# Performance work log

Hardware: AMD Instinct MI355X
Metric: run time of the kernel (lower is better)

## Reference

```python
import jax, jax.numpy as jnp
import numpy as np

# Model dims (match init_kwargs)
B, S, IN = 8, 96, 128          # batch, seq_len, control+data bits
H, M, N = 2, 32, 512           # heads, memory content size, memory addresses
STATE, OUT, NS = 256, 126, 3   # hidden state, output (data bits), shift size
EPS = 1e-12
# per-head interface parameter layout: s, jd, j, gamma, erase, add, k, beta, g
_SPLITS = [NS, 1, 3, 1, M, M, M, 1, 1]
_OFFS = np.concatenate([[0], np.cumsum(_SPLITS)])


def setup_inputs() -> dict:
    key = jax.random.key(0)
    ks = jax.random.split(key, 4)
    CIN = IN + H * M + STATE  # controller input: x ++ read ++ state
    return {
        "x": jax.random.normal(ks[0], (B, S, IN), jnp.float32),
        "W_s": jax.random.normal(ks[1], (CIN, STATE), jnp.float32) * 0.05,
        "b_s": jnp.zeros((STATE,), jnp.float32),
        "W_o": jax.random.normal(ks[2], (CIN, OUT), jnp.float32) * 0.05,
        "b_o": jnp.zeros((OUT,), jnp.float32),
        "W_u": jax.random.normal(ks[3], (CIN, int(_OFFS[-1]) * H), jnp.float32) * 0.05,
        "b_u": jnp.zeros((int(_OFFS[-1]) * H,), jnp.float32),
    }


def _circular_conv(wt, s):
    # wt: [B,H,N], s: [B,H,NS] softmax shift kernel centered at 0
    out = jnp.zeros_like(wt)
    c = NS // 2
    for i in range(NS):
        out = out + s[..., i:i + 1] * jnp.roll(wt, shift=i - c, axis=-1)
    return out


def _dwm_forward(x, W_s, b_s, W_o, b_o, W_u, b_u):
    b = x.shape[0]
    state0 = jnp.ones((b, STATE), x.dtype)
    wt0 = jnp.zeros((b, H, N), x.dtype).at[:, :, 0].set(1.0)
    mem0 = jnp.full((b, M, N), 0.01, x.dtype)

    def step(carry, x_t):
        state, wt, wt_dyn, mem = carry
        # ---- read: attention over memory addresses ----
        read = jnp.einsum('bhn,bmn->bhm', wt, mem).reshape(b, H * M)
        comb = jnp.concatenate([x_t, read, state], axis=-1)
        # ---- controller ----
        state_n = jax.nn.sigmoid(comb @ W_s + b_s)
        out_t = comb @ W_o + b_o
        upd = (comb @ W_u + b_u).reshape(b, H, int(_OFFS[-1]))
        sp = [upd[..., int(_OFFS[i]):int(_OFFS[i + 1])] for i in range(len(_SPLITS))]
        s, jd, j, gamma, erase, add, k, beta, g = sp
        s = jax.nn.softmax(jax.nn.softplus(s), axis=-1)
        jd = jax.nn.sigmoid(jd)
        j = jax.nn.softmax(j, axis=-1)
        gamma = 1.0 + jax.nn.softplus(gamma)
        erase = jax.nn.sigmoid(erase)
        k = jnp.tanh(k)
        beta = jax.nn.softplus(beta)
        g = jax.nn.sigmoid(g)
        # ---- memory write (erase then add, NTM-style multi-head) ----
        mem = mem * jnp.prod(1.0 - erase[:, :, :, None] * wt[:, :, None, :], axis=1)
        mem = mem + jnp.einsum('bhm,bhn->bmn', add, wt)
        # ---- content addressing (cosine similarity) ----
        k_n = k / (jnp.linalg.norm(k, axis=-1, keepdims=True) + EPS)
        m_n = mem / (jnp.linalg.norm(mem, axis=1, keepdims=True) + EPS)
        wt_k = jnp.einsum('bhm,bmn->bhn', k_n, m_n)
        wt_c = g * jax.nn.softmax(beta * wt_k, axis=-1) + (1.0 - g) * wt
        # ---- shift + sharpen + renormalize ----
        wt_sh = (_circular_conv(wt_c, s) + EPS) ** gamma
        wt_n = wt_sh / jnp.sum(wt_sh, axis=-1, keepdims=True)
        # ---- bookmark (snapshot) update + jump interpolation ----
        wt_a0 = jnp.zeros_like(wt_n).at[..., 0].set(1.0)
        wt_dyn_n = (1.0 - jd) * wt_dyn + jd * wt_n
        wt_f = j[..., 0:1] * wt_n + j[..., 1:2] * wt_a0 + j[..., 2:3] * wt_dyn
        return (state_n, wt_f, wt_dyn_n, mem), out_t

    _, outs = jax.lax.scan(step, (state0, wt0, wt0, mem0), jnp.swapaxes(x, 0, 1))
    return jnp.swapaxes(outs, 0, 1)  # [B, S, OUT]


def reference(x, W_s, b_s, W_o, b_o, W_u, b_u):
    return _dwm_forward(x, W_s, b_s, W_o, b_o, W_u, b_u)
```

## Files before the change

### kernel.cpp

```cpp
#include <hip/hip_runtime.h>
#include <math.h>

#define NTHREADS 1024

namespace {
constexpr int kB = 8, kS = 96, kIN = 128, kH = 2, kM = 32, kN = 512;
constexpr int kSTATE = 256, kOUT = 126, kUH = 106;
constexpr int kNC = 594;
constexpr int kKR = 320;
constexpr int kMLD = 520;
constexpr float kEPS = 1e-12f;
constexpr int kXWfloats = kB * kS * kNC;
constexpr size_t kWbOffBytes = (size_t)kXWfloats * 4;
}

__device__ __forceinline__ float sigm_(float x) { return 1.0f / (1.0f + __expf(-x)); }
__device__ __forceinline__ float splus_(float x) { return x > 20.0f ? x : __logf(1.0f + __expf(x)); }
__device__ __forceinline__ float blo_(unsigned int u) { return __uint_as_float(u << 16); }
__device__ __forceinline__ float bhi_(unsigned int u) { return __uint_as_float(u & 0xffff0000u); }

__global__ __launch_bounds__(640) void prep_xw(
    const float* __restrict__ x,
    const float* __restrict__ Ws, const float* __restrict__ bs,
    const float* __restrict__ Wo, const float* __restrict__ bo,
    const float* __restrict__ Wu, const float* __restrict__ bu,
    float* __restrict__ xw)
{
    __shared__ float sx[kIN];
    const int row = blockIdx.x;
    const int t = threadIdx.x;
    if (t < kIN) sx[t] = x[row * kIN + t];
    __syncthreads();
    if (t < kNC) {
        const float* Wp; int ld, j; float acc;
        if (t < 256)      { Wp = Ws; ld = kSTATE;   j = t;       acc = bs[j]; }
        else if (t < 382) { Wp = Wo; ld = kOUT;     j = t - 256; acc = bo[j]; }
        else              { Wp = Wu; ld = kH * kUH; j = t - 382; acc = bu[j]; }
        const float* p = Wp + j;
        #pragma unroll 8
        for (int i = 0; i < kIN; ++i) acc = fmaf(sx[i], p[i * ld], acc);
        xw[row * kNC + t] = acc;
    }
}

__global__ __launch_bounds__(1024) void prep_pack(
    const float* __restrict__ Ws, const float* __restrict__ Wo,
    const float* __restrict__ Wu, unsigned short* __restrict__ Wb)
{
    int idx = blockIdx.x * 1024 + threadIdx.x;
    if (idx >= kKR * kNC) return;
    int i = idx / kNC, c = idx - i * kNC;
    float v;
    if (c < 256)      v = Ws[(kIN + i) * kSTATE + c];
    else if (c < 382) v = Wo[(kIN + i) * kOUT + (c - 256)];
    else              v = Wu[(kIN + i) * (kH * kUH) + (c - 382)];
    unsigned int bits = __float_as_uint(v);
    unsigned int r = (bits + 0x7fffu + ((bits >> 16) & 1u)) >> 16;
    Wb[idx] = (unsigned short)r;
}

__global__ __launch_bounds__(NTHREADS) void dwm_kernel(
    const float* __restrict__ xw,
    const unsigned int* __restrict__ Wb,
    float* __restrict__ out)
{
    __shared__ float s_mem[kM * kMLD];
    __shared__ float s_wt[kH * kN];
    __shared__ float s_wtd[kH * kN];
    __shared__ float s_tmp[kH * kN];
    __shared__ float s_comb[320];
    __shared__ float s_upd[kH * kUH];
    __shared__ float s_er[kH * kM], s_ad[kH * kM], s_kk[kH * kM];
    __shared__ float s_red[16];
    __shared__ float s_shift[kH][3], s_jmp[kH][3];
    __shared__ float s_jd[kH], s_gam[kH], s_beta[kH], s_g[kH], s_ikn[kH];

    const int b = blockIdx.x;
    const int t = threadIdx.x;
    const int wid = t >> 6;
    const int lane = t & 63;

    for (int i = t; i < kM * kN; i += NTHREADS)
        s_mem[(i >> 9) * kMLD + (i & 511)] = 0.01f;
    for (int i = t; i < kH * kN; i += NTHREADS) {
        float v = ((i & 511) == 0) ? 1.0f : 0.0f;
        s_wt[i] = v; s_wtd[i] = v;
    }
    if (t < kSTATE) s_comb[64 + t] = 1.0f;
    __syncthreads();

    for (int step = 0; step < kS; ++step) {
        {
            int g = t >> 4, l16 = t & 15, h = g >> 5, m = g & 31;
            const float4* w4 = (const float4*)&s_wt[h * kN];
            const float4* m4 = (const float4*)&s_mem[m * kMLD];
            float ax = 0.0f, ay = 0.0f, az = 0.0f, aw = 0.0f;
            #pragma unroll
            for (int k = 0; k < 8; ++k) {
                float4 w = w4[l16 + 16 * k];
                float4 mv = m4[l16 + 16 * k];
                ax = fmaf(w.x, mv.x, ax); ay = fmaf(w.y, mv.y, ay);
                az = fmaf(w.z, mv.z, az); aw = fmaf(w.w, mv.w, aw);
            }
            float acc = (ax + ay) + (az + aw);
            acc += __shfl_xor(acc, 1);
            acc += __shfl_xor(acc, 2);
            acc += __shfl_xor(acc, 4);
            acc += __shfl_xor(acc, 8);
            if (l16 == 0) s_comb[g] = acc;
        }
        __syncthreads();

        float a0 = 0.0f, a1 = 0.0f;
        if (t < 297) {
            const unsigned int* wp = Wb + t;
            const float* xr = &xw[(b * kS + step) * kNC + 2 * t];
            a0 = xr[0]; a1 = xr[1];
            #pragma unroll 16
            for (int i = 0; i < kKR; ++i) {
                unsigned int u = wp[i * 297];
                float c = s_comb[i];
                a0 = fmaf(blo_(u), c, a0);
                a1 = fmaf(bhi_(u), c, a1);
            }
        }
        __syncthreads();

        if (t < 297) {
            int c0 = 2 * t;
            if (c0 < kSTATE) {
                s_comb[64 + c0] = sigm_(a0);
                s_comb[65 + c0] = sigm_(a1);
            } else if (c0 < kSTATE + kOUT) {
                float* o = &out[(b * kS + step) * kOUT];
                o[c0 - 256] = a0; o[c0 - 255] = a1;
            } else {
                int i0 = c0 - 382;
                auto disp = [&](int idx, float v) {
                    int h = idx >= kUH;
                    int j = idx - (h ? kUH : 0);
                    if (j >= 8 && j < 40)        s_er[h * kM + j - 8]  = sigm_(v);
                    else if (j >= 40 && j < 72)  s_ad[h * kM + j - 40] = v;
                    else if (j >= 72 && j < 104) s_kk[h * kM + j - 72] = tanhf(v);
                    else s_upd[idx] = v;
                };
                disp(i0, a0);
                disp(i0 + 1, a1);
            }
        }
        __syncthreads();

        if (t < 64) {
            int h = t >> 5, m = t & 31;
            float kv = s_kk[t];
            float ss = kv * kv;
            ss += __shfl_xor(ss, 1);
            ss += __shfl_xor(ss, 2);
            ss += __shfl_xor(ss, 4);
            ss += __shfl_xor(ss, 8);
            ss += __shfl_xor(ss, 16);
            if (m == 0) s_ikn[h] = 1.0f / (sqrtf(ss) + kEPS);
        } else if (t == 64 || t == 65) {
            int h = t - 64;
            const float* u = &s_upd[h * kUH];
            float b0 = splus_(u[0]), b1 = splus_(u[1]), b2 = splus_(u[2]);
            float mx = fmaxf(b0, fmaxf(b1, b2));
            float e0 = __expf(b0 - mx), e1 = __expf(b1 - mx), e2 = __expf(b2 - mx);
            float inv = 1.0f / (e0 + e1 + e2);
            s_shift[h][0] = e0 * inv; s_shift[h][1] = e1 * inv; s_shift[h][2] = e2 * inv;
            s_jd[h] = sigm_(u[3]);
            b0 = u[4]; b1 = u[5]; b2 = u[6];
            mx = fmaxf(b0, fmaxf(b1, b2));
            e0 = __expf(b0 - mx); e1 = __expf(b1 - mx); e2 = __expf(b2 - mx);
            inv = 1.0f / (e0 + e1 + e2);
            s_jmp[h][0] = e0 * inv; s_jmp[h][1] = e1 * inv; s_jmp[h][2] = e2 * inv;
            s_gam[h]  = 1.0f + splus_(u[7]);
            s_beta[h] = splus_(u[104]);
            s_g[h]    = sigm_(u[105]);
        }
        {
            int tn = t & 127, tm = t >> 7;
            int n0 = tn << 2;
            float4 w0v = *(const float4*)&s_wt[n0];
            float4 w1v = *(const float4*)&s_wt[kN + n0];
            #pragma unroll
            for (int r = 0; r < 4; ++r) {
                int m = tm + (r << 3);
                float er0 = s_er[m], er1 = s_er[kM + m];
                float ad0 = s_ad[m], ad1 = s_ad[kM + m];
                float4* mp = (float4*)&s_mem[m * kMLD + n0];
                float4 v = *mp;
                v.x = v.x * (1.0f - er0 * w0v.x) * (1.0f - er1 * w1v.x) + ad0 * w0v.x + ad1 * w1v.x;
                v.y = v.y * (1.0f - er0 * w0v.y) * (1.0f - er1 * w1v.y) + ad0 * w0v.y + ad1 * w1v.y;
                v.z = v.z * (1.0f - er0 * w0v.z) * (1.0f - er1 * w1v.z) + ad0 * w0v.z + ad1 * w1v.z;
                v.w = v.w * (1.0f - er0 * w0v.w) * (1.0f - er1 * w1v.w) + ad0 * w0v.w + ad1 * w1v.w;
                *mp = v;
            }
        }
        __syncthreads();

        if (t < kN) {
            int n = t;
            float c0 = 0.0f, c1 = 0.0f, ss = 0.0f;
            #pragma unroll
            for (int m = 0; m < kM; ++m) {
                float v = s_mem[m * kMLD + n];
                c0 = fmaf(s_kk[m], v, c0);
                c1 = fmaf(s_kk[kM + m], v, c1);
                ss = fmaf(v, v, ss);
            }
            float invc = 1.0f / (sqrtf(ss) + kEPS);
            float e0 = __expf(s_beta[0] * (c0 * s_ikn[0] * invc));
            float e1 = __expf(s_beta[1] * (c1 * s_ikn[1] * invc));
            s_tmp[n]      = e0;
            s_tmp[kN + n] = e1;
            float sm0 = e0, sm1 = e1;
            sm0 += __shfl_xor(sm0, 1);  sm1 += __shfl_xor(sm1, 1);
            sm0 += __shfl_xor(sm0, 2);  sm1 += __shfl_xor(sm1, 2);
            sm0 += __shfl_xor(sm0, 4);  sm1 += __shfl_xor(sm1, 4);
            sm0 += __shfl_xor(sm0, 8);  sm1 += __shfl_xor(sm1, 8);
            sm0 += __shfl_xor(sm0, 16); sm1 += __shfl_xor(sm1, 16);
            sm0 += __shfl_xor(sm0, 32); sm1 += __shfl_xor(sm1, 32);
            if (lane == 0) { s_red[wid] = sm0; s_red[8 + wid] = sm1; }
        }
        __syncthreads();

        {
            int h = t >> 9;
            float tot = 0.0f;
            #pragma unroll
            for (int i = 0; i < 8; ++i) tot += s_red[h * 8 + i];
            float e = s_tmp[t];
            float wc = s_g[h] * e / tot + (1.0f - s_g[h]) * s_wt[t];
            s_tmp[t] = wc;
        }
        __syncthreads();

        {
            int h = t >> 9, n = t & 511;
            const float* wcp = &s_tmp[h * kN];
            float cv = s_shift[h][0] * wcp[(n + 1) & 511]
                     + s_shift[h][1] * wcp[n]
                     + s_shift[h][2] * wcp[(n + 511) & 511];
            float wsh = exp2f(s_gam[h] * __log2f(cv + kEPS));
            float sm = wsh;
            sm += __shfl_xor(sm, 1);
            sm += __shfl_xor(sm, 2);
            sm += __shfl_xor(sm, 4);
            sm += __shfl_xor(sm, 8);
            sm += __shfl_xor(sm, 16);
            sm += __shfl_xor(sm, 32);
            if (lane == 0) s_red[wid] = sm;
            __syncthreads();
            float tot = 0.0f;
            #pragma unroll
            for (int i = 0; i < 8; ++i) tot += s_red[h * 8 + i];
            float wn = wsh / tot;
            float dold = s_wtd[t];
            s_wtd[t] = (1.0f - s_jd[h]) * dold + s_jd[h] * wn;
            float wa0 = (n == 0) ? 1.0f : 0.0f;
            s_wt[t] = s_jmp[h][0] * wn + s_jmp[h][1] * wa0 + s_jmp[h][2] * dold;
        }
        __syncthreads();
    }
}

extern "C" void kernel_launch(void* const* d_in, const int* in_sizes, int n_in,
                              void* d_out, int out_size, void* d_ws, size_t ws_size,
                              hipStream_t stream) {
    const float* x   = (const float*)d_in[0];
    const float* Ws  = (const float*)d_in[1];
    const float* bs  = (const float*)d_in[2];
    const float* Wo  = (const float*)d_in[3];
    const float* bo  = (const float*)d_in[4];
    const float* Wu  = (const float*)d_in[5];
    const float* bu  = (const float*)d_in[6];
    float* outp = (float*)d_out;

    float* xw = (float*)d_ws;
    unsigned short* Wb = (unsigned short*)((char*)d_ws + kWbOffBytes);

    prep_xw<<<dim3(kB * kS), dim3(640), 0, stream>>>(x, Ws, bs, Wo, bo, Wu, bu, xw);
    prep_pack<<<dim3((kKR * kNC + 1023) / 1024), dim3(1024), 0, stream>>>(Ws, Wo, Wu, Wb);
    dwm_kernel<<<dim3(kB), dim3(NTHREADS), 0, stream>>>(xw, (const unsigned int*)Wb, outp);
}
```

Measured before the change: 1.010 ms.

## Cache first weight rows in LDS and double-buffer comb to drop a barrier

The first 64 rows of the packed bf16 controller weights are loaded into shared memory once per block, and the per-step matvec reads them from LDS instead of global memory. The comb vector is double-buffered so new state can be written without the barrier that used to separate the matvec from the writeback. This cuts global and L2 traffic on the serial recurrence and removes one sync per step. In exchange it uses about 76KB more LDS, and two split accumulators slightly change the summation order.

```diff
diff --git a/kernel.cpp b/kernel.cpp
--- a/kernel.cpp
+++ b/kernel.cpp
@@ -8,6 +8,7 @@
 constexpr int kSTATE = 256, kOUT = 126, kUH = 106;
 constexpr int kNC = 594;
 constexpr int kKR = 320;
+constexpr int kLC = 64;
 constexpr int kMLD = 520;
 constexpr float kEPS = 1e-12f;
 constexpr int kXWfloats = kB * kS * kNC;
@@ -65,10 +66,11 @@
     float* __restrict__ out)
 {
     __shared__ float s_mem[kM * kMLD];
+    __shared__ unsigned int s_wc[kLC * 297];
     __shared__ float s_wt[kH * kN];
     __shared__ float s_wtd[kH * kN];
     __shared__ float s_tmp[kH * kN];
-    __shared__ float s_comb[320];
+    __shared__ float s_comb[2][320];
     __shared__ float s_upd[kH * kUH];
     __shared__ float s_er[kH * kM], s_ad[kH * kM], s_kk[kH * kM];
     __shared__ float s_red[16];
@@ -80,15 +82,17 @@
     const int wid = t >> 6;
     const int lane = t & 63;
 
+    for (int i = t; i < kLC * 297; i += NTHREADS) s_wc[i] = Wb[i];
     for (int i = t; i < kM * kN; i += NTHREADS)
         s_mem[(i >> 9) * kMLD + (i & 511)] = 0.01f;
     for (int i = t; i < kH * kN; i += NTHREADS) {
         float v = ((i & 511) == 0) ? 1.0f : 0.0f;
         s_wt[i] = v; s_wtd[i] = v;
     }
-    if (t < kSTATE) s_comb[64 + t] = 1.0f;
+    if (t < kSTATE) s_comb[0][64 + t] = 1.0f;
     __syncthreads();
 
+    int p = 0;
     for (int step = 0; step < kS; ++step) {
         {
             int g = t >> 4, l16 = t & 15, h = g >> 5, m = g & 31;
@@ -107,30 +111,36 @@
             acc += __shfl_xor(acc, 2);
             acc += __shfl_xor(acc, 4);
             acc += __shfl_xor(acc, 8);
-            if (l16 == 0) s_comb[g] = acc;
-        }
-        __syncthreads();
-
-        float a0 = 0.0f, a1 = 0.0f;
+            if (l16 == 0) s_comb[p][g] = acc;
+        }
+        __syncthreads();
+
         if (t < 297) {
-            const unsigned int* wp = Wb + t;
+            const float* cb = s_comb[p];
             const float* xr = &xw[(b * kS + step) * kNC + 2 * t];
-            a0 = xr[0]; a1 = xr[1];
+            float a0 = xr[0], a1 = xr[1];
+            float l0 = 0.0f, l1 = 0.0f;
+            #pragma unroll 8
+            for (int i = 0; i < kLC; ++i) {
+                unsigned int u = s_wc[i * 297 + t];
+                float c = cb[i];
+                l0 = fmaf(blo_(u), c, l0);
+                l1 = fmaf(bhi_(u), c, l1);
+            }
+            const unsigned int* wp = Wb + kLC * 297 + t;
             #pragma unroll 16
-            for (int i = 0; i < kKR; ++i) {
+            for (int i = 0; i < kKR - kLC; ++i) {
                 unsigned int u = wp[i * 297];
-                float c = s_comb[i];
+                float c = cb[kLC + i];
                 a0 = fmaf(blo_(u), c, a0);
                 a1 = fmaf(bhi_(u), c, a1);
             }
-        }
-        __syncthreads();
-
-        if (t < 297) {
+            a0 += l0; a1 += l1;
+
             int c0 = 2 * t;
             if (c0 < kSTATE) {
-                s_comb[64 + c0] = sigm_(a0);
-                s_comb[65 + c0] = sigm_(a1);
+                s_comb[p ^ 1][64 + c0] = sigm_(a0);
+                s_comb[p ^ 1][65 + c0] = sigm_(a1);
             } else if (c0 < kSTATE + kOUT) {
                 float* o = &out[(b * kS + step) * kOUT];
                 o[c0 - 256] = a0; o[c0 - 255] = a1;
@@ -262,6 +272,7 @@
             s_wt[t] = s_jmp[h][0] * wn + s_jmp[h][1] * wa0 + s_jmp[h][2] * dold;
         }
         __syncthreads();
+        p ^= 1;
     }
 }
 
```

Result: slower. 2.830 ms (+180.1%).

## Overlap memory read with state-part of controller matvec using double-buffered comb

Applied to the files above, without the earlier changes.

The read dot-product over memory now runs on threads 512-1023 at the same time as threads 0-296 accumulate the controller matvec over the state rows (64..319). The remaining 64 read rows are accumulated after a barrier. The combined-input buffer is double-buffered so the new state can be written without racing the ongoing reads. This removes one barrier and lets the read phase hide behind the weight-streaming loop, at the cost of a split loop and extra shared memory.

```diff
diff --git a/kernel.cpp b/kernel.cpp
--- a/kernel.cpp
+++ b/kernel.cpp
@@ -68,7 +68,7 @@
     __shared__ float s_wt[kH * kN];
     __shared__ float s_wtd[kH * kN];
     __shared__ float s_tmp[kH * kN];
-    __shared__ float s_comb[320];
+    __shared__ float s_comb[2][320];
     __shared__ float s_upd[kH * kUH];
     __shared__ float s_er[kH * kM], s_ad[kH * kM], s_kk[kH * kM];
     __shared__ float s_red[16];
@@ -86,51 +86,59 @@
         float v = ((i & 511) == 0) ? 1.0f : 0.0f;
         s_wt[i] = v; s_wtd[i] = v;
     }
-    if (t < kSTATE) s_comb[64 + t] = 1.0f;
+    if (t < kSTATE) s_comb[0][64 + t] = 1.0f;
     __syncthreads();
 
+    int p = 0;
     for (int step = 0; step < kS; ++step) {
-        {
-            int g = t >> 4, l16 = t & 15, h = g >> 5, m = g & 31;
-            const float4* w4 = (const float4*)&s_wt[h * kN];
-            const float4* m4 = (const float4*)&s_mem[m * kMLD];
-            float ax = 0.0f, ay = 0.0f, az = 0.0f, aw = 0.0f;
-            #pragma unroll
-            for (int k = 0; k < 8; ++k) {
-                float4 w = w4[l16 + 16 * k];
-                float4 mv = m4[l16 + 16 * k];
-                ax = fmaf(w.x, mv.x, ax); ay = fmaf(w.y, mv.y, ay);
-                az = fmaf(w.z, mv.z, az); aw = fmaf(w.w, mv.w, aw);
-            }
-            float acc = (ax + ay) + (az + aw);
-            acc += __shfl_xor(acc, 1);
-            acc += __shfl_xor(acc, 2);
-            acc += __shfl_xor(acc, 4);
-            acc += __shfl_xor(acc, 8);
-            if (l16 == 0) s_comb[g] = acc;
-        }
-        __syncthreads();
-
         float a0 = 0.0f, a1 = 0.0f;
         if (t < 297) {
             const unsigned int* wp = Wb + t;
             const float* xr = &xw[(b * kS + step) * kNC + 2 * t];
             a0 = xr[0]; a1 = xr[1];
+            const float* cb = s_comb[p];
             #pragma unroll 16
-            for (int i = 0; i < kKR; ++i) {
+            for (int i = 64; i < kKR; ++i) {
                 unsigned int u = wp[i * 297];
-                float c = s_comb[i];
+                float c = cb[i];
                 a0 = fmaf(blo_(u), c, a0);
                 a1 = fmaf(bhi_(u), c, a1);
             }
+        } else if (t >= 512) {
+            int tt = t - 512;
+            int g = tt >> 3, l8 = tt & 7, h = g >> 5, m = g & 31;
+            const float4* w4 = (const float4*)&s_wt[h * kN];
+            const float4* m4 = (const float4*)&s_mem[m * kMLD];
+            float ax = 0.0f, ay = 0.0f, az = 0.0f, aw = 0.0f;
+            #pragma unroll
+            for (int k = 0; k < 16; ++k) {
+                float4 w = w4[l8 + 8 * k];
+                float4 mv = m4[l8 + 8 * k];
+                ax = fmaf(w.x, mv.x, ax); ay = fmaf(w.y, mv.y, ay);
+                az = fmaf(w.z, mv.z, az); aw = fmaf(w.w, mv.w, aw);
+            }
+            float r = (ax + ay) + (az + aw);
+            r += __shfl_xor(r, 1);
+            r += __shfl_xor(r, 2);
+            r += __shfl_xor(r, 4);
+            if (l8 == 0) s_comb[p][g] = r;
         }
         __syncthreads();
 
         if (t < 297) {
+            const unsigned int* wp = Wb + t;
+            const float* cb = s_comb[p];
+            #pragma unroll 16
+            for (int i = 0; i < 64; ++i) {
+                unsigned int u = wp[i * 297];
+                float c = cb[i];
+                a0 = fmaf(blo_(u), c, a0);
+                a1 = fmaf(bhi_(u), c, a1);
+            }
             int c0 = 2 * t;
             if (c0 < kSTATE) {
-                s_comb[64 + c0] = sigm_(a0);
-                s_comb[65 + c0] = sigm_(a1);
+                s_comb[p ^ 1][64 + c0] = sigm_(a0);
+                s_comb[p ^ 1][65 + c0] = sigm_(a1);
             } else if (c0 < kSTATE + kOUT) {
                 float* o = &out[(b * kS + step) * kOUT];
                 o[c0 - 256] = a0; o[c0 - 255] = a1;
@@ -262,6 +270,7 @@
             s_wt[t] = s_jmp[h][0] * wn + s_jmp[h][1] * wa0 + s_jmp[h][2] * dold;
         }
         __syncthreads();
+        p ^= 1;
     }
 }
 
```

Result: slower. 2.824 ms (+179.6%).
